# Kernel tuning notes

Hardware: AMD Instinct MI355X
Metric: run time of the kernel (lower is better)

Reference implementation:

```python
import jax, jax.numpy as jnp
import numpy as np

NEG_SLOPE = 0.2  # PyG RGATConv default negative_slope


def _rgat_conv(x, src, dst, edge_type, W, q, k, b, num_nodes):
    # W: [R, in, H] per-relation weight (heads=1 so H = heads*out_channels)
    # Transform every node by every relation once, then gather per edge
    # (same math as PyG's per-edge bmm with index_select'd weights, but
    #  avoids materializing [E, in, H] weights).
    xr = jnp.einsum('ni,rio->rno', x, W)            # [R, N, H]
    qv = jnp.einsum('rno,oh->rnh', xr, q)           # [R, N, heads]
    kv = jnp.einsum('rno,oh->rnh', xr, k)           # [R, N, heads]
    # additive self-attention: alpha_e = leaky_relu(q(out_i) + k(out_j))
    alpha = qv[edge_type, dst] + kv[edge_type, src]  # [E, heads]
    alpha = jnp.where(alpha >= 0, alpha, NEG_SLOPE * alpha)
    # softmax over incoming edges of each destination node (across-relation)
    amax = jax.ops.segment_max(alpha, dst, num_segments=num_nodes)  # [N, heads]
    amax = jnp.where(jnp.isfinite(amax), amax, 0.0)
    ex = jnp.exp(alpha - amax[dst])
    denom = jax.ops.segment_sum(ex, dst, num_segments=num_nodes)
    att = ex / (denom[dst] + 1e-16)                 # [E, heads]
    msg = xr[edge_type, src] * att                  # [E, H] (heads=1 broadcast)
    out = jax.ops.segment_sum(msg, dst, num_segments=num_nodes)    # [N, H]
    return out + b


def setup_inputs() -> dict:
    key = jax.random.key(0)
    ks = jax.random.split(key, 16)
    N, E, R, IN, H = 50000, 800000, 8, 128, 128
    x = jax.random.normal(ks[0], (N, IN), dtype=jnp.float32)
    edge_index = jax.random.randint(ks[1], (2, E), 0, N, dtype=jnp.int32)
    edge_type = jax.random.randint(ks[2], (E,), 0, R, dtype=jnp.int32)
    s_in = 1.0 / np.sqrt(IN)
    s_h = 1.0 / np.sqrt(H)
    w0 = jax.random.normal(ks[3], (R, IN, H), dtype=jnp.float32) * s_in
    q0 = jax.random.normal(ks[4], (H, 1), dtype=jnp.float32) * s_h
    k0 = jax.random.normal(ks[5], (H, 1), dtype=jnp.float32) * s_h
    b0 = jnp.zeros((H,), dtype=jnp.float32)
    w1 = jax.random.normal(ks[6], (R, H, H), dtype=jnp.float32) * s_h
    q1 = jax.random.normal(ks[7], (H, 1), dtype=jnp.float32) * s_h
    k1 = jax.random.normal(ks[8], (H, 1), dtype=jnp.float32) * s_h
    b1 = jnp.zeros((H,), dtype=jnp.float32)
    fc1_w = jax.random.normal(ks[9], (2 * H, H), dtype=jnp.float32) * (1.0 / np.sqrt(2 * H))
    fc1_b = jnp.zeros((H,), dtype=jnp.float32)
    fc2_w = jax.random.normal(ks[10], (H, 1), dtype=jnp.float32) * s_h
    fc2_b = jnp.zeros((1,), dtype=jnp.float32)
    return {"x": x, "edge_index": edge_index, "edge_type": edge_type,
            "w0": w0, "q0": q0, "k0": k0, "b0": b0,
            "w1": w1, "q1": q1, "k1": k1, "b1": b1,
            "fc1_w": fc1_w, "fc1_b": fc1_b, "fc2_w": fc2_w, "fc2_b": fc2_b}


def reference(x, edge_index, edge_type, w0, q0, k0, b0, w1, q1, k1, b1, fc1_w, fc1_b, fc2_w, fc2_b):
    N = x.shape[0]
    src, dst = edge_index[0], edge_index[1]
    h = jax.nn.relu(_rgat_conv(x, src, dst, edge_type, w0, q0, k0, b0, N))
    h = jax.nn.relu(_rgat_conv(h, src, dst, edge_type, w1, q1, k1, b1, N))
    g = jnp.concatenate([h.mean(axis=0), h.max(axis=0)], axis=-1)  # [2H]
    g = jnp.tanh(g)
    g = jax.nn.relu(g @ fc1_w + fc1_b)   # dropout is identity in eval mode
    out = g @ fc2_w + fc2_b              # [1]
    return jax.nn.sigmoid(out)
```

## Files before the change

kernel.cpp:

```cpp
#include <hip/hip_runtime.h>
#include <hip/hip_bf16.h>


typedef __bf16 bf16x8 __attribute__((ext_vector_type(8)));
typedef __bf16 bf16x4 __attribute__((ext_vector_type(4)));
typedef __bf16 bf16x2 __attribute__((ext_vector_type(2)));
typedef float f32x4 __attribute__((ext_vector_type(4)));
typedef float f32x2 __attribute__((ext_vector_type(2)));

#define CBSH 10
#define CSC_CH 4096


__global__ __launch_bounds__(256) void k_chist(const int* __restrict__ dst, int* __restrict__ chist, int E) {
  __shared__ int lh[64];
  int t = threadIdx.x;
  if (t < 64) lh[t] = 0;
  __syncthreads();
  for (int e = blockIdx.x * 256 + t; e < E; e += gridDim.x * 256)
    atomicAdd(&lh[dst[e] >> CBSH], 1);
  __syncthreads();
  if (t < 64 && lh[t]) atomicAdd(&chist[t], lh[t]);
}

__global__ __launch_bounds__(256) void k_cscatter(const int* __restrict__ src, const int* __restrict__ dst,
                                                  const int* __restrict__ et, const int* __restrict__ chist,
                                                  int* __restrict__ ccur0, int* __restrict__ tmp, int E) {
  __shared__ int recbuf[CSC_CH];
  __shared__ int lcnt[64], lbase[64], gbase[64], lcur[64], cb[64];
  int t = threadIdx.x;
  int base = blockIdx.x * CSC_CH;
  int cnt = E - base; if (cnt > CSC_CH) cnt = CSC_CH;
  if (t < 64) { lcnt[t] = 0; cb[t] = chist[t]; }
  __syncthreads();
  int myrec[CSC_CH / 256], mycb[CSC_CH / 256];
  int k = 0;
  for (int i = t; i < cnt; i += 256, ++k) {
    int d = dst[base + i];
    int c = d >> CBSH;
    myrec[k] = src[base + i] | (et[base + i] << 17) | ((d & ((1 << CBSH) - 1)) << 20);
    mycb[k] = c;
    atomicAdd(&lcnt[c], 1);
  }
  __syncthreads();
  if (t == 0) {
    int acc = 0, acc2 = 0;
    for (int c = 0; c < 64; ++c) {
      lbase[c] = acc; lcur[c] = acc; acc += lcnt[c];
      int h = cb[c]; cb[c] = acc2; acc2 += h;
    }
  }
  __syncthreads();
  if (t < 64 && lcnt[t] > 0) gbase[t] = cb[t] + atomicAdd(&ccur0[t], lcnt[t]);
  __syncthreads();
  k = 0;
  for (int i = t; i < cnt; i += 256, ++k) {
    int p = atomicAdd(&lcur[mycb[k]], 1);
    recbuf[p] = myrec[k];
  }
  __syncthreads();
  for (int i = t; i < cnt; i += 256) {
    int lo = 0, hi = 63;
    while (lo < hi) { int mid = (lo + hi + 1) >> 1; if (lbase[mid] <= i) lo = mid; else hi = mid - 1; }
    tmp[gbase[lo] + (i - lbase[lo])] = recbuf[i];
  }
}

__global__ __launch_bounds__(1024) void k_fsort(const int* __restrict__ chist, const int* __restrict__ tmp,
                                                int* __restrict__ recs, int* __restrict__ row_ptr,
                                                int N, int E) {
  __shared__ int sd[1024];
  __shared__ int ncur[1024];
  __shared__ int cbs[65];
  int cb = blockIdx.x, t = threadIdx.x;
  int n0 = cb << CBSH;
  if (t < 64) cbs[t] = chist[t];
  __syncthreads();
  if (t == 0) {
    int acc = 0;
    for (int c = 0; c < 64; ++c) { int h = cbs[c]; cbs[c] = acc; acc += h; }
    cbs[64] = acc;
  }
  sd[t] = 0;
  __syncthreads();
  int begin = cbs[cb], endd = cbs[cb + 1];
  for (int i = begin + t; i < endd; i += 1024)
    atomicAdd(&sd[(tmp[i] >> 20) & 1023], 1);
  __syncthreads();
  int myc = sd[t];
  for (int off = 1; off < 1024; off <<= 1) {
    int xv = 0; if (t >= off) xv = sd[t - off];
    __syncthreads();
    sd[t] += xv;
    __syncthreads();
  }
  int ex = sd[t] - myc;
  int node = n0 + t;
  if (node < N) row_ptr[node] = begin + ex;
  if (node == N - 1) row_ptr[N] = E;
  ncur[t] = begin + ex;
  __syncthreads();
  for (int i = begin + t; i < endd; i += 1024) {
    int rc = tmp[i];
    int p = atomicAdd(&ncur[(rc >> 20) & 1023], 1);
    recs[p] = rc & 0xFFFFF;
  }
}


__global__ __launch_bounds__(256) void k_wprep(const float* __restrict__ w0, const float* __restrict__ q0,
                                               const float* __restrict__ k0, const float* __restrict__ w1,
                                               const float* __restrict__ q1, const float* __restrict__ k1,
                                               __bf16* __restrict__ wqkb, __bf16* __restrict__ WT) {
  int layer = blockIdx.x >> 9;
  int bx = blockIdx.x;
  if (bx >= 384) { layer = 1; bx -= 384; } else layer = 0;
  const float* W = layer ? w1 : w0;
  const float* q = layer ? q1 : q0;
  const float* k = layer ? k1 : k0;
  __bf16* wq = wqkb + layer * 2048;
  __bf16* WTl = WT + (size_t)layer * 131072;
  if (bx < 256) {
    int g = bx * 4 + (threadIdx.x >> 6);
    int lane = threadIdx.x & 63;
    const float2* wrow = (const float2*)(W + (size_t)g * 128);
    float2 wv = wrow[lane];
    float2 qv2 = ((const float2*)q)[lane];
    float2 kv2 = ((const float2*)k)[lane];
    float aq = wv.x * qv2.x + wv.y * qv2.y;
    float ak = wv.x * kv2.x + wv.y * kv2.y;
    #pragma unroll
    for (int off = 32; off; off >>= 1) {
      aq += __shfl_xor(aq, off, 64);
      ak += __shfl_xor(ak, off, 64);
    }
    if (lane == 0) { wq[g] = (__bf16)aq; wq[1024 + g] = (__bf16)ak; }
  } else {
    __shared__ float t[32][33];
    int bb = bx - 256;
    int r = bb >> 4;
    int rem = bb & 15;
    int kk0 = (rem & 3) * 32, h0 = (rem >> 2) * 32;
    int tx = threadIdx.x & 31;
    int ty = threadIdx.x >> 5;
    #pragma unroll
    for (int i = 0; i < 4; ++i) {
      int kk = ty + i * 8;
      t[kk][tx] = W[((size_t)r * 128 + kk0 + kk) * 128 + h0 + tx];
    }
    __syncthreads();
    #pragma unroll
    for (int i = 0; i < 4; ++i) {
      int hh = ty + i * 8;
      WTl[(size_t)(h0 + hh) * 1024 + r * 128 + kk0 + tx] = (__bf16)t[tx][hh];
    }
  }
}


#define ASTR 136

template <int L0>
__global__ __launch_bounds__(256) void k_gemmY(const void* __restrict__ xin,
                                               const __bf16* __restrict__ WT2,
                                               const __bf16* __restrict__ wqkb,
                                               unsigned char* __restrict__ Y, float* __restrict__ qkv, int M) {
  __shared__ __bf16 As[128 * ASTR];
  __shared__ __bf16 Bs[128 * ASTR];
  int bm = blockIdx.x * 128;
  int tid = threadIdx.x;
  int w = tid >> 6, l = tid & 63;
  int srow = tid >> 1;
  int cb8 = (tid & 1) * 8;
  bool valid = (bm + srow) < M;

  if (L0) {
    const float* gA = (const float*)xin + (size_t)(bm + srow) * 128 + cb8 * 8;
    #pragma unroll
    for (int i = 0; i < 8; ++i) {
      float4 f0 = make_float4(0.f, 0.f, 0.f, 0.f), f1 = f0;
      if (valid) { f0 = *(const float4*)(gA + i * 8); f1 = *(const float4*)(gA + i * 8 + 4); }
      bf16x8 v;
      v[0] = (__bf16)f0.x; v[1] = (__bf16)f0.y; v[2] = (__bf16)f0.z; v[3] = (__bf16)f0.w;
      v[4] = (__bf16)f1.x; v[5] = (__bf16)f1.y; v[6] = (__bf16)f1.z; v[7] = (__bf16)f1.w;
      *(bf16x8*)&As[srow * ASTR + (cb8 + i) * 8] = v;
    }
  } else {
    const bf16x8* gA = (const bf16x8*)((const __bf16*)xin + (size_t)(bm + srow) * 128);
    #pragma unroll
    for (int i = 0; i < 8; ++i) {
      bf16x8 v = valid ? gA[cb8 + i] : (bf16x8)(__bf16)0.0f;
      *(bf16x8*)&As[srow * ASTR + (cb8 + i) * 8] = v;
    }
  }
  {
    int qr = tid >> 4, qc = tid & 15;
    *(bf16x8*)&Bs[qr * ASTR + qc * 8] = *(const bf16x8*)(wqkb + (size_t)qr * 128 + qc * 8);
  }
  __syncthreads();

  {
    f32x4 qacc[2];
    qacc[0] = (f32x4)0.f; qacc[1] = (f32x4)0.f;
    #pragma unroll
    for (int ks = 0; ks < 4; ++ks) {
      bf16x8 bq = *(const bf16x8*)&Bs[(l & 15) * ASTR + ks * 32 + (l >> 4) * 8];
      #pragma unroll
      for (int m2 = 0; m2 < 2; ++m2) {
        bf16x8 af = *(const bf16x8*)&As[(w * 32 + m2 * 16 + (l & 15)) * ASTR + ks * 32 + (l >> 4) * 8];
        qacc[m2] = __builtin_amdgcn_mfma_f32_16x16x32_bf16(af, bq, qacc[m2], 0, 0, 0);
      }
    }
    #pragma unroll
    for (int m2 = 0; m2 < 2; ++m2)
      #pragma unroll
      for (int j = 0; j < 4; ++j) {
        int row = w * 32 + m2 * 16 + (l >> 4) * 4 + j;
        if (bm + row < M) qkv[(size_t)(bm + row) * 16 + (l & 15)] = qacc[m2][j];
      }
  }

  for (int r = 0; r < 8; ++r) {
    __syncthreads();
    {
      const bf16x8* gB = (const bf16x8*)(WT2 + (size_t)srow * 1024 + r * 128);
      #pragma unroll
      for (int i = 0; i < 8; ++i)
        *(bf16x8*)&Bs[srow * ASTR + (cb8 + i) * 8] = gB[cb8 + i];
    }
    __syncthreads();

    f32x4 acc[2][8];
    #pragma unroll
    for (int m2 = 0; m2 < 2; ++m2)
      #pragma unroll
      for (int n2 = 0; n2 < 8; ++n2) acc[m2][n2] = (f32x4)0.f;

    #pragma unroll
    for (int ks = 0; ks < 4; ++ks) {
      bf16x8 af[2], bfv[8];
      #pragma unroll
      for (int m2 = 0; m2 < 2; ++m2)
        af[m2] = *(const bf16x8*)&As[(w * 32 + m2 * 16 + (l & 15)) * ASTR + ks * 32 + (l >> 4) * 8];
      #pragma unroll
      for (int n2 = 0; n2 < 8; ++n2)
        bfv[n2] = *(const bf16x8*)&Bs[(n2 * 16 + (l & 15)) * ASTR + ks * 32 + (l >> 4) * 8];
      #pragma unroll
      for (int m2 = 0; m2 < 2; ++m2)
        #pragma unroll
        for (int n2 = 0; n2 < 8; ++n2)
          acc[m2][n2] = __builtin_amdgcn_mfma_f32_16x16x32_bf16(af[m2], bfv[n2], acc[m2][n2], 0, 0, 0);
    }

    unsigned char* Yr = Y + ((size_t)r * M + bm) * 128;
    #pragma unroll
    for (int m2 = 0; m2 < 2; ++m2)
      #pragma unroll
      for (int j = 0; j < 4; ++j) {
        int row = w * 32 + m2 * 16 + (l >> 4) * 4 + j;
        if (bm + row < M) {
          #pragma unroll
          for (int n2 = 0; n2 < 8; ++n2) {
            float v = acc[m2][n2][j];
            int pk = __builtin_amdgcn_cvt_pk_fp8_f32(v, v, 0, false);
            Yr[(size_t)row * 128 + n2 * 16 + (l & 15)] = (unsigned char)(pk & 0xFF);
          }
        }
      }
  }
}


__global__ __launch_bounds__(256) void k_aggY(const int* __restrict__ row_ptr, const int* __restrict__ recs,
                                              const float* __restrict__ qkv, const unsigned char* __restrict__ Y,
                                              const float* __restrict__ bias, __bf16* __restrict__ hout,
                                              int N) {
  int wv = threadIdx.x >> 6;
  int lane = threadIdx.x & 63;
  int n = blockIdx.x * 4 + wv;
  if (n >= N) return;
  int start = row_ptr[n], end = row_ptr[n + 1];
  const float* qvn = qkv + (size_t)n * 16;
  float denom = 0.f, m_run = -1e30f;
  int sub = lane & 15;
  int grp = lane >> 4;
  float acc[8];
  #pragma unroll
  for (int j = 0; j < 8; ++j) acc[j] = 0.f;

  for (int c0 = start; c0 < end; c0 += 64) {
    int cend = (end < c0 + 64) ? end : (c0 + 64);
    int cnt = cend - c0;
    int p = c0 + lane;
    float a = -1e30f; int rec = 0;
    if (p < cend) {
      rec = recs[p];
      int s = rec & 0x1FFFF, r = (rec >> 17) & 7;
      float t = qvn[r] + qkv[(size_t)s * 16 + 8 + r];
      a = (t >= 0.f) ? t : 0.2f * t;
    }
    float cm = a;
    #pragma unroll
    for (int off = 32; off; off >>= 1) cm = fmaxf(cm, __shfl_xor(cm, off, 64));
    if (cm > m_run) {
      if (m_run > -1e29f) {
        float scale = __expf(m_run - cm);
        denom *= scale;
        #pragma unroll
        for (int j = 0; j < 8; ++j) acc[j] *= scale;
      }
      m_run = cm;
    }
    float wgt = (p < cend) ? __expf(a - m_run) : 0.f;
    float ws = wgt;
    #pragma unroll
    for (int off = 32; off; off >>= 1) ws += __shfl_xor(ws, off, 64);
    denom += ws;
    int wbits = __float_as_int(wgt);

    int nbatch = (cnt + 3) >> 2;
    #pragma unroll 2
    for (int b = 0; b < nbatch; ++b) {
      int idx = grp * 4 + b * 16;
      int rg = __builtin_amdgcn_ds_bpermute(idx, rec);
      int wg = __builtin_amdgcn_ds_bpermute(idx, wbits);
      float fw = __int_as_float(wg);
      int s_ = rg & 0x1FFFF;
      int r_ = (rg >> 17) & 7;
      int2 xv = *(const int2*)(Y + (((size_t)r_ * N + s_) << 7) + sub * 8);
      f32x2 f01 = __builtin_amdgcn_cvt_pk_f32_fp8(xv.x, false);
      f32x2 f23 = __builtin_amdgcn_cvt_pk_f32_fp8(xv.x, true);
      f32x2 f45 = __builtin_amdgcn_cvt_pk_f32_fp8(xv.y, false);
      f32x2 f67 = __builtin_amdgcn_cvt_pk_f32_fp8(xv.y, true);
      acc[0] += fw * f01[0]; acc[1] += fw * f01[1];
      acc[2] += fw * f23[0]; acc[3] += fw * f23[1];
      acc[4] += fw * f45[0]; acc[5] += fw * f45[1];
      acc[6] += fw * f67[0]; acc[7] += fw * f67[1];
    }
  }

  #pragma unroll
  for (int j = 0; j < 8; ++j) {
    acc[j] += __shfl_xor(acc[j], 16, 64);
    acc[j] += __shfl_xor(acc[j], 32, 64);
  }
  float inv = 1.f / (denom + 1e-16f);
  if (grp == 0) {
    float4 b0 = *(const float4*)(bias + sub * 8);
    float4 b1 = *(const float4*)(bias + sub * 8 + 4);
    float bb[8] = {b0.x, b0.y, b0.z, b0.w, b1.x, b1.y, b1.z, b1.w};
    bf16x8 o;
    #pragma unroll
    for (int j = 0; j < 8; ++j) o[j] = (__bf16)fmaxf(acc[j] * inv + bb[j], 0.f);
    *(bf16x8*)(hout + (size_t)n * 128 + sub * 8) = o;
  }
}


__global__ __launch_bounds__(256) void k_pool(const __bf16* __restrict__ h, float* __restrict__ gsum,
                                              float* __restrict__ gmax, int N) {
  int c2 = threadIdx.x & 63;
  int grp = threadIdx.x >> 6;
  float s0 = 0.f, s1 = 0.f, m0 = 0.f, m1 = 0.f;
  for (int n = blockIdx.x * 4 + grp; n < N; n += gridDim.x * 4) {
    bf16x2 v = ((const bf16x2*)(h + (size_t)n * 128))[c2];
    float v0 = (float)v.x, v1 = (float)v.y;
    s0 += v0; s1 += v1;
    m0 = fmaxf(m0, v0); m1 = fmaxf(m1, v1);
  }
  __shared__ float ss0[256], ss1[256], sm0[256], sm1[256];
  ss0[threadIdx.x] = s0; ss1[threadIdx.x] = s1;
  sm0[threadIdx.x] = m0; sm1[threadIdx.x] = m1;
  __syncthreads();
  if (grp == 0) {
    #pragma unroll
    for (int g = 1; g < 4; ++g) {
      s0 += ss0[g * 64 + c2]; s1 += ss1[g * 64 + c2];
      m0 = fmaxf(m0, sm0[g * 64 + c2]); m1 = fmaxf(m1, sm1[g * 64 + c2]);
    }
    atomicAdd(&gsum[2 * c2 + 0], s0);
    atomicAdd(&gsum[2 * c2 + 1], s1);
    atomicMax((int*)gmax + 2 * c2 + 0, __float_as_int(m0));
    atomicMax((int*)gmax + 2 * c2 + 1, __float_as_int(m1));
  }
}

__global__ void k_head(const float* __restrict__ gsum, const float* __restrict__ gmax,
                       const float* __restrict__ fc1w, const float* __restrict__ fc1b,
                       const float* __restrict__ fc2w, const float* __restrict__ fc2b,
                       float* __restrict__ out, int N) {
  __shared__ float g[256];
  __shared__ float red[128];
  int t = threadIdx.x;
  if (t < 128) g[t] = tanhf(gsum[t] / (float)N);
  else g[t] = tanhf(gmax[t - 128]);
  __syncthreads();
  float r1 = 0.f;
  if (t < 128) {
    float a = fc1b[t];
    for (int i = 0; i < 256; i++) a += g[i] * fc1w[i * 128 + t];
    r1 = a > 0.f ? a : 0.f;
    red[t] = r1 * fc2w[t];
  }
  __syncthreads();
  for (int s = 64; s > 0; s >>= 1) {
    if (t < s) red[t] += red[t + s];
    __syncthreads();
  }
  if (t == 0) {
    float o = red[0] + fc2b[0];
    out[0] = 1.f / (1.f + __expf(-o));
  }
}


extern "C" void kernel_launch(void* const* d_in, const int* in_sizes, int n_in,
                              void* d_out, int out_size, void* d_ws, size_t ws_size,
                              hipStream_t stream) {
  const float* x    = (const float*)d_in[0];
  const int*   ei   = (const int*)d_in[1];
  const int*   ety  = (const int*)d_in[2];
  const float* w0   = (const float*)d_in[3];
  const float* q0   = (const float*)d_in[4];
  const float* k0   = (const float*)d_in[5];
  const float* b0   = (const float*)d_in[6];
  const float* w1   = (const float*)d_in[7];
  const float* q1   = (const float*)d_in[8];
  const float* k1   = (const float*)d_in[9];
  const float* b1   = (const float*)d_in[10];
  const float* fc1w = (const float*)d_in[11];
  const float* fc1b = (const float*)d_in[12];
  const float* fc2w = (const float*)d_in[13];
  const float* fc2b = (const float*)d_in[14];
  int N = in_sizes[0] / 128;
  int E = in_sizes[2];
  const int* src = ei;
  const int* dst = ei + E;

  char* base = (char*)d_ws;
  size_t off = 0;
  auto alloc = [&](size_t bytes) -> void* {
    off = (off + 255) & ~(size_t)255;
    void* p = base + off;
    off += bytes;
    return p;
  };
  int ncb = (N + (1 << CBSH) - 1) >> CBSH;

  int*    row_ptr = (int*)alloc((size_t)(N + 1) * 4);
  int*    ctrl    = (int*)alloc(384 * 4);
  int*    chist   = ctrl;
  int*    ccur0   = ctrl + 64;
  float*  gpool   = (float*)(ctrl + 128);
  float*  gsum    = gpool;
  float*  gmax    = gpool + 128;
  int*    tmp     = (int*)alloc((size_t)E * 4);
  int*    recs    = (int*)alloc((size_t)E * 4);
  float*  qkv     = (float*)alloc((size_t)N * 16 * 4);
  __bf16* wqkb    = (__bf16*)alloc(2 * 2048 * 2);
  __bf16* h1b     = (__bf16*)alloc((size_t)N * 128 * 2);
  __bf16* h2b     = (__bf16*)alloc((size_t)N * 128 * 2);
  __bf16* WT2     = (__bf16*)alloc((size_t)2 * 131072 * 2);
  unsigned char* Y = (unsigned char*)alloc((size_t)8 * N * 128);

  hipMemsetAsync(ctrl, 0, 384 * 4, stream);
  k_chist<<<256, 256, 0, stream>>>(dst, chist, E);
  k_cscatter<<<(E + CSC_CH - 1) / CSC_CH, 256, 0, stream>>>(src, dst, ety, chist, ccur0, tmp, E);
  k_fsort<<<ncb, 1024, 0, stream>>>(chist, tmp, recs, row_ptr, N, E);

  k_wprep<<<768, 256, 0, stream>>>(w0, q0, k0, w1, q1, k1, wqkb, WT2);

  for (int layer = 0; layer < 2; ++layer) {
    const float* bb   = layer ? b1 : b0;
    __bf16*      hout = layer ? h2b : h1b;
    if (layer == 0)
      k_gemmY<1><<<(N + 127) / 128, 256, 0, stream>>>((const void*)x, WT2, wqkb, Y, qkv, N);
    else
      k_gemmY<0><<<(N + 127) / 128, 256, 0, stream>>>((const void*)h1b, WT2 + 131072, wqkb + 2048, Y, qkv, N);
    k_aggY<<<(N + 3) / 4, 256, 0, stream>>>(row_ptr, recs, qkv, Y, bb, hout, N);
  }

  k_pool<<<256, 256, 0, stream>>>(h2b, gsum, gmax, N);
  k_head<<<1, 256, 0, stream>>>(gsum, gmax, fc1w, fc1b, fc2w, fc2b, (float*)d_out, N);
}
```

Baseline: 242.3 us.

## Keep A fragments in registers, share one LDS buffer, pack fp8 stores

The A tile is loaded from LDS into registers once, so a single shared buffer can be reused for both A and B, halving LDS use. The MFMA operands are swapped so that each lane's accumulator holds four consecutive output columns of one row. Those four values are then packed into one 32-bit fp8 store instead of four byte stores. The aim is to raise occupancy, remove repeated A reads from LDS, and coalesce the Y writes, at the cost of 32 extra VGPRs for the A fragments.

```diff
diff --git a/kernel.cpp b/kernel.cpp
--- a/kernel.cpp
+++ b/kernel.cpp
@@ -112,8 +112,7 @@
                                                const float* __restrict__ k0, const float* __restrict__ w1,
                                                const float* __restrict__ q1, const float* __restrict__ k1,
                                                __bf16* __restrict__ wqkb, __bf16* __restrict__ WT) {
-  int layer = blockIdx.x >> 9;
-  int bx = blockIdx.x;
+  int layer, bx = blockIdx.x;
   if (bx >= 384) { layer = 1; bx -= 384; } else layer = 0;
   const float* W = layer ? w1 : w0;
   const float* q = layer ? q1 : q0;
@@ -165,8 +164,7 @@
                                                const __bf16* __restrict__ WT2,
                                                const __bf16* __restrict__ wqkb,
                                                unsigned char* __restrict__ Y, float* __restrict__ qkv, int M) {
-  __shared__ __bf16 As[128 * ASTR];
-  __shared__ __bf16 Bs[128 * ASTR];
+  __shared__ __bf16 Sbuf[128 * ASTR];
   int bm = blockIdx.x * 128;
   int tid = threadIdx.x;
   int w = tid >> 6, l = tid & 63;
@@ -183,33 +181,40 @@
       bf16x8 v;
       v[0] = (__bf16)f0.x; v[1] = (__bf16)f0.y; v[2] = (__bf16)f0.z; v[3] = (__bf16)f0.w;
       v[4] = (__bf16)f1.x; v[5] = (__bf16)f1.y; v[6] = (__bf16)f1.z; v[7] = (__bf16)f1.w;
-      *(bf16x8*)&As[srow * ASTR + (cb8 + i) * 8] = v;
+      *(bf16x8*)&Sbuf[srow * ASTR + (cb8 + i) * 8] = v;
     }
   } else {
     const bf16x8* gA = (const bf16x8*)((const __bf16*)xin + (size_t)(bm + srow) * 128);
     #pragma unroll
     for (int i = 0; i < 8; ++i) {
       bf16x8 v = valid ? gA[cb8 + i] : (bf16x8)(__bf16)0.0f;
-      *(bf16x8*)&As[srow * ASTR + (cb8 + i) * 8] = v;
-    }
-  }
+      *(bf16x8*)&Sbuf[srow * ASTR + (cb8 + i) * 8] = v;
+    }
+  }
+  __syncthreads();
+
+  bf16x8 afr[2][4];
+  #pragma unroll
+  for (int m2 = 0; m2 < 2; ++m2)
+    #pragma unroll
+    for (int ks = 0; ks < 4; ++ks)
+      afr[m2][ks] = *(const bf16x8*)&Sbuf[(w * 32 + m2 * 16 + (l & 15)) * ASTR + ks * 32 + (l >> 4) * 8];
+  __syncthreads();
+
   {
     int qr = tid >> 4, qc = tid & 15;
-    *(bf16x8*)&Bs[qr * ASTR + qc * 8] = *(const bf16x8*)(wqkb + (size_t)qr * 128 + qc * 8);
-  }
-  __syncthreads();
-
+    *(bf16x8*)&Sbuf[qr * ASTR + qc * 8] = *(const bf16x8*)(wqkb + (size_t)qr * 128 + qc * 8);
+  }
+  __syncthreads();
   {
     f32x4 qacc[2];
     qacc[0] = (f32x4)0.f; qacc[1] = (f32x4)0.f;
     #pragma unroll
     for (int ks = 0; ks < 4; ++ks) {
-      bf16x8 bq = *(const bf16x8*)&Bs[(l & 15) * ASTR + ks * 32 + (l >> 4) * 8];
-      #pragma unroll
-      for (int m2 = 0; m2 < 2; ++m2) {
-        bf16x8 af = *(const bf16x8*)&As[(w * 32 + m2 * 16 + (l & 15)) * ASTR + ks * 32 + (l >> 4) * 8];
-        qacc[m2] = __builtin_amdgcn_mfma_f32_16x16x32_bf16(af, bq, qacc[m2], 0, 0, 0);
-      }
+      bf16x8 bq = *(const bf16x8*)&Sbuf[(l & 15) * ASTR + ks * 32 + (l >> 4) * 8];
+      #pragma unroll
+      for (int m2 = 0; m2 < 2; ++m2)
+        qacc[m2] = __builtin_amdgcn_mfma_f32_16x16x32_bf16(afr[m2][ks], bq, qacc[m2], 0, 0, 0);
     }
     #pragma unroll
     for (int m2 = 0; m2 < 2; ++m2)
@@ -220,13 +225,17 @@
       }
   }
 
+  int arow[2];
+  #pragma unroll
+  for (int m2 = 0; m2 < 2; ++m2) arow[m2] = w * 32 + m2 * 16 + (l & 15);
+
   for (int r = 0; r < 8; ++r) {
     __syncthreads();
     {
       const bf16x8* gB = (const bf16x8*)(WT2 + (size_t)srow * 1024 + r * 128);
       #pragma unroll
       for (int i = 0; i < 8; ++i)
-        *(bf16x8*)&Bs[srow * ASTR + (cb8 + i) * 8] = gB[cb8 + i];
+        *(bf16x8*)&Sbuf[srow * ASTR + (cb8 + i) * 8] = gB[cb8 + i];
     }
     __syncthreads();
 
@@ -238,35 +247,29 @@
 
     #pragma unroll
     for (int ks = 0; ks < 4; ++ks) {
-      bf16x8 af[2], bfv[8];
-      #pragma unroll
-      for (int m2 = 0; m2 < 2; ++m2)
-        af[m2] = *(const bf16x8*)&As[(w * 32 + m2 * 16 + (l & 15)) * ASTR + ks * 32 + (l >> 4) * 8];
+      bf16x8 bfv[8];
       #pragma unroll
       for (int n2 = 0; n2 < 8; ++n2)
-        bfv[n2] = *(const bf16x8*)&Bs[(n2 * 16 + (l & 15)) * ASTR + ks * 32 + (l >> 4) * 8];
+        bfv[n2] = *(const bf16x8*)&Sbuf[(n2 * 16 + (l & 15)) * ASTR + ks * 32 + (l >> 4) * 8];
       #pragma unroll
       for (int m2 = 0; m2 < 2; ++m2)
         #pragma unroll
         for (int n2 = 0; n2 < 8; ++n2)
-          acc[m2][n2] = __builtin_amdgcn_mfma_f32_16x16x32_bf16(af[m2], bfv[n2], acc[m2][n2], 0, 0, 0);
+          acc[m2][n2] = __builtin_amdgcn_mfma_f32_16x16x32_bf16(bfv[n2], afr[m2][ks], acc[m2][n2], 0, 0, 0);
     }
 
     unsigned char* Yr = Y + ((size_t)r * M + bm) * 128;
     #pragma unroll
-    for (int m2 = 0; m2 < 2; ++m2)
-      #pragma unroll
-      for (int j = 0; j < 4; ++j) {
-        int row = w * 32 + m2 * 16 + (l >> 4) * 4 + j;
-        if (bm + row < M) {
-          #pragma unroll
-          for (int n2 = 0; n2 < 8; ++n2) {
-            float v = acc[m2][n2][j];
-            int pk = __builtin_amdgcn_cvt_pk_fp8_f32(v, v, 0, false);
-            Yr[(size_t)row * 128 + n2 * 16 + (l & 15)] = (unsigned char)(pk & 0xFF);
-          }
+    for (int m2 = 0; m2 < 2; ++m2) {
+      if (bm + arow[m2] < M) {
+        #pragma unroll
+        for (int n2 = 0; n2 < 8; ++n2) {
+          int pk = __builtin_amdgcn_cvt_pk_fp8_f32(acc[m2][n2][0], acc[m2][n2][1], 0, false);
+          pk = __builtin_amdgcn_cvt_pk_fp8_f32(acc[m2][n2][2], acc[m2][n2][3], pk, true);
+          *(int*)(Yr + (size_t)arow[m2] * 128 + n2 * 16 + (l >> 4) * 4) = pk;
         }
       }
+    }
   }
 }
 
```

Measured after the change: 274.7 us. 1.13x slower.
